# Kernel optimization log

Hardware: AMD Instinct MI355X
Metric: run time of the kernel (lower is better)

Reference implementation:

```python
import jax, jax.numpy as jnp
import numpy as np

P = 16            # patch_size
D = 256           # hidden_dim == P*P (required by final reshape)
H = 8             # num_heads
HD = D // H       # head_dim


def _sinusoid(n, d):
    # standard sinusoidal positional encoding, interleaved sin/cos
    pos = jnp.arange(n, dtype=jnp.float32)[:, None]            # (n,1)
    i = jnp.arange(0, d, 2, dtype=jnp.float32)                 # (d/2,)
    div = jnp.exp(-i * (jnp.log(10000.0) / d))                 # (d/2,)
    ang = pos * div                                            # (n, d/2)
    return jnp.stack([jnp.sin(ang), jnp.cos(ang)], axis=-1).reshape(n, d)


def _patch_embed(x, w, b):
    # Conv2d(in_ch, D, kernel=P, stride=P) then flatten to (B, N, D)
    e = jax.lax.conv_general_dilated(
        x, w, window_strides=(P, P), padding='VALID',
        dimension_numbers=('NCHW', 'OIHW', 'NCHW'))
    e = e + b[None, :, None, None]
    B = e.shape[0]
    e = e.reshape(B, D, -1).transpose(0, 2, 1)                 # (B, N, D)
    e = e + _sinusoid(e.shape[1], D)[None]                     # positional enc
    return e.reshape(B, -1, H, HD).transpose(0, 2, 1, 3)       # (B, H, N, HD)


def setup_inputs() -> dict:
    key = jax.random.key(0)
    ks = jax.random.split(key, 12)
    B = 16
    inp = {
        'q': jax.random.normal(ks[0], (B, 3, 512, 512), jnp.float32),
        'k': jax.random.normal(ks[1], (B, 3, 512, 512), jnp.float32),
        'v': jax.random.normal(ks[2], (B, 3, 512, 512), jnp.float32),
        'a': jax.random.normal(ks[3], (B, 3, 256, 256), jnp.float32),
    }
    s = 0.02
    for idx, name in enumerate('qkva'):
        inp['w' + name] = jax.random.normal(ks[4 + 2 * idx], (D, 3, P, P), jnp.float32) * s
        inp['b' + name] = jnp.zeros((D,), jnp.float32)
    return inp


def reference(q, k, v, a, wq, bq, wk, bk, wv, bv, wa, ba):
    qh = _patch_embed(q, wq, bq)   # (B,H,Nq,HD), Nq=1024
    kh = _patch_embed(k, wk, bk)   # (B,H,Nk,HD)
    vh = _patch_embed(v, wv, bv)   # (B,H,Nk,HD)
    ah = _patch_embed(a, wa, ba)   # (B,H,Na,HD), Na=256
    scale = HD ** -0.5
    # agent attention: two small softmax matmuls then Q @ (K @ V)
    Qs = jax.nn.softmax(jnp.einsum('bhnd,bhmd->bhnm', qh, ah) * scale, axis=-1)  # (B,H,Nq,Na)
    Ks = jax.nn.softmax(jnp.einsum('bhmd,bhnd->bhmn', ah, kh) * scale, axis=-1)  # (B,H,Na,Nk)
    KV = jnp.einsum('bhmn,bhnd->bhmd', Ks, vh)                                   # (B,H,Na,HD)
    A = jnp.einsum('bhnm,bhmd->bhnd', Qs, KV)                                    # (B,H,Nq,HD)
    B = A.shape[0]
    attn = A.transpose(0, 2, 1, 3).reshape(B, -1, D)            # (B, Nq, D)
    N = attn.shape[1]
    g = int(N ** 0.5)                                           # grid side (32)
    HW = g * P                                                  # 512
    attn = attn.reshape(B, N, P, P)
    attn = attn.reshape(B, g, g, P, P).transpose(0, 1, 3, 2, 4).reshape(B, HW, HW)
    return attn
```

## Files before the change

kernel.cpp:

```cpp
#include <hip/hip_runtime.h>
#include <cstdint>
#include <cstddef>

typedef __bf16 bf16x8 __attribute__((ext_vector_type(8)));
typedef __bf16 bf16x4 __attribute__((ext_vector_type(4)));
typedef float f32x4 __attribute__((ext_vector_type(4)));
typedef unsigned short u16x4 __attribute__((ext_vector_type(4)));
typedef unsigned short u16x8 __attribute__((ext_vector_type(8)));

#define MFMA16(a, b, c) __builtin_amdgcn_mfma_f32_16x16x32_bf16(a, b, c, 0, 0, 0)

__device__ __forceinline__ unsigned short f2bf(float f) {
    unsigned u = __builtin_bit_cast(unsigned, f);
    u = (u + 0x7FFFu + ((u >> 16) & 1u)) >> 16;
    return (unsigned short)u;
}

__global__ __launch_bounds__(256)
void prep(float* __restrict__ pe, unsigned short* __restrict__ Wb,
          const float* __restrict__ w0, const float* __restrict__ w1,
          const float* __restrict__ w2, const float* __restrict__ w3) {
    const int bx = blockIdx.x, t = threadIdx.x;
    if (bx < 1024) {
        int n = bx, d = t;
        int j = d >> 1;
        float div = expf(-(float)(2 * j) * 0.03597789207808881f);
        float ang = (float)n * div;
        pe[n * 256 + d] = (d & 1) ? cosf(ang) : sinf(ang);
    } else {
        int i = bx - 1024;
        int tensor = i / 192, blk = i - tensor * 192;
        const float* w = (tensor == 0) ? w0 : (tensor == 1) ? w1 : (tensor == 2) ? w2 : w3;
        int idx4 = blk * 256 + t;
        int d = idx4 / 192;
        int kq = (idx4 - d * 192) * 4;
        f32x4 v = *(const f32x4*)(w + (size_t)idx4 * 4);
        u16x4 o;
#pragma unroll
        for (int e = 0; e < 4; ++e) o[e] = f2bf(v[e]);
        unsigned short* dst = Wb + (size_t)tensor * 196608
                            + (d >> 4) * 12288 + (kq >> 5) * 512
                            + (d & 15) * 32 + (kq & 31);
        *(u16x4*)dst = o;
    }
}

struct EArgs {
    const float* src;
    const unsigned short* Wb;
    const float* bias;
    const float* pe;
    unsigned short* dst;
    int Np, lgNp, lgG, S, trans;
};

template<bool TR>
__device__ __forceinline__ void embed_body(const EArgs& A, int m0) {
    const int t = threadIdx.x, lane = t & 63, wid = t >> 6;
    const int l15 = lane & 15, l4 = lane >> 4;
    const int S = A.S;

    const float* pbase[4];
    int nn[4], bb[4];
#pragma unroll
    for (int j = 0; j < 4; ++j) {
        int p = m0 + j * 16 + l15;
        int b = p >> A.lgNp, n = p & (A.Np - 1);
        nn[j] = n; bb[j] = b;
        int gy = n >> A.lgG, gx = n & ((1 << A.lgG) - 1);
        pbase[j] = A.src + ((size_t)(b * 3) * S + gy * 16 + (l4 >> 1)) * (size_t)S
                 + gx * 16 + (l4 & 1) * 8;
    }
    const unsigned short* wbase = A.Wb + (size_t)(wid * 4) * 12288 + l15 * 32 + l4 * 8;

    f32x4 acc[4][4];
#pragma unroll
    for (int i = 0; i < 4; ++i)
#pragma unroll
        for (int j = 0; j < 4; ++j) acc[i][j] = f32x4{0.f, 0.f, 0.f, 0.f};

    for (int kt = 0; kt < 24; ++kt) {
        const size_t aoff = ((size_t)(kt >> 3) * S + (kt & 7) * 2) * (size_t)S;
        bf16x8 pf[4], wf[4];
#pragma unroll
        for (int j = 0; j < 4; ++j) {
            f32x4 lo = *(const f32x4*)(pbase[j] + aoff);
            f32x4 hi = *(const f32x4*)(pbase[j] + aoff + 4);
            bf16x8 v;
#pragma unroll
            for (int e = 0; e < 4; ++e) { v[e] = (__bf16)lo[e]; v[4 + e] = (__bf16)hi[e]; }
            pf[j] = v;
        }
#pragma unroll
        for (int i = 0; i < 4; ++i)
            wf[i] = *(const bf16x8*)(wbase + i * 12288 + kt * 512);
#pragma unroll
        for (int i = 0; i < 4; ++i)
#pragma unroll
            for (int j = 0; j < 4; ++j) {
                if (TR) acc[i][j] = MFMA16(pf[i], wf[j], acc[i][j]);
                else    acc[i][j] = MFMA16(wf[i], pf[j], acc[i][j]);
            }
    }

    if (!TR) {
#pragma unroll
        for (int i = 0; i < 4; ++i) {
            int d0 = wid * 64 + i * 16 + l4 * 4;
            int hh = d0 >> 5, hd = d0 & 31;
            f32x4 bs = *(const f32x4*)&A.bias[d0];
#pragma unroll
            for (int j = 0; j < 4; ++j) {
                int n = nn[j], b = bb[j];
                f32x4 pv = *(const f32x4*)&A.pe[n * 256 + d0];
                bf16x4 o;
#pragma unroll
                for (int r = 0; r < 4; ++r)
                    o[r] = (__bf16)(acc[i][j][r] + bs[r] + pv[r]);
                *(bf16x4*)&A.dst[(((size_t)(b * 8 + hh)) * A.Np + n) * 32 + hd] = o;
            }
        }
    } else {
#pragma unroll
        for (int j = 0; j < 4; ++j) {
            int d = wid * 64 + j * 16 + l15;
            int hh = d >> 5, hd = d & 31;
            float bsv = A.bias[d];
#pragma unroll
            for (int i = 0; i < 4; ++i) {
                int p0 = m0 + i * 16 + l4 * 4;
                int b = p0 >> A.lgNp, n0 = p0 & (A.Np - 1);
                bf16x4 o;
#pragma unroll
                for (int r = 0; r < 4; ++r)
                    o[r] = (__bf16)(acc[i][j][r] + bsv + A.pe[(n0 + r) * 256 + d]);
                *(bf16x4*)&A.dst[(((size_t)(b * 8 + hh)) * 32 + hd) * (size_t)A.Np + n0] = o;
            }
        }
    }
}

__global__ __launch_bounds__(256, 3)
void embed2(EArgs A0, EArgs A1, EArgs A2, EArgs A3) {
    const int bx = blockIdx.x;
    EArgs A; int m0;
    if      (bx < 256) { A = A0; m0 = bx * 64; }
    else if (bx < 512) { A = A1; m0 = (bx - 256) * 64; }
    else if (bx < 768) { A = A2; m0 = (bx - 512) * 64; }
    else               { A = A3; m0 = (bx - 768) * 64; }
    if (A.trans) embed_body<true>(A, m0);
    else         embed_body<false>(A, m0);
}

__global__ __launch_bounds__(512)
void s2kv_kernel(const unsigned short* __restrict__ ah_ws,
                 const unsigned short* __restrict__ kh_ws,
                 const unsigned short* __restrict__ vT_ws,
                 unsigned short* __restrict__ kvT_ws) {
    __shared__ unsigned short ahs[128][40];
    __shared__ unsigned short khs[128][40];
    __shared__ unsigned short vts[32][136];
    __shared__ unsigned short Ps[128][136];

    const int bid = blockIdx.x;
    const int half = bid & 1;
    const int h = (bid >> 1) & 7, b = bid >> 4;
    const int a0 = half * 128;
    const int t = threadIdx.x, lane = t & 63, wid = t >> 6;
    const int l15 = lane & 15, l4 = lane >> 4;
    const size_t bh = (size_t)(b * 8 + h);

    const unsigned short* ahp = ah_ws + (bh * 256 + a0) * 32;
    const unsigned short* khp = kh_ws + bh * 1024 * 32;
    const unsigned short* vtp = vT_ws + bh * 32 * 1024;

    {
        int row = t >> 2, kq = (t & 3) * 8;
        *(u16x8*)&ahs[row][kq] = *(const u16x8*)(ahp + row * 32 + kq);
    }
    __syncthreads();
    const bf16x8 af = *(const bf16x8*)&ahs[wid * 16 + l15][l4 * 8];

    const float scale = 0.17677669529663687f;
    float rs[4] = {0.f, 0.f, 0.f, 0.f};
    const f32x4 z = {0.f, 0.f, 0.f, 0.f};
    f32x4 kv[2];
    kv[0] = z; kv[1] = z;

    for (int kt = 0; kt < 8; ++kt) {
        const int n0 = kt * 128;
        __syncthreads();
        {
            int row = t >> 2, kq = (t & 3) * 8;
            *(u16x8*)&khs[row][kq] = *(const u16x8*)(khp + (size_t)(n0 + row) * 32 + kq);
        }
        {
            int row = t >> 4, cq = (t & 15) * 8;
            *(u16x8*)&vts[row][cq] = *(const u16x8*)(vtp + (size_t)row * 1024 + n0 + cq);
        }
        __syncthreads();
#pragma unroll
        for (int n16 = 0; n16 < 8; ++n16) {
            bf16x8 bfr = *(const bf16x8*)&khs[n16 * 16 + l15][l4 * 8];
            f32x4 s = MFMA16(af, bfr, z);
#pragma unroll
            for (int r = 0; r < 4; ++r) {
                float e = __expf(s[r] * scale);
                rs[r] += e;
                Ps[wid * 16 + l4 * 4 + r][n16 * 16 + l15] = f2bf(e);
            }
        }
        __syncthreads();
#pragma unroll
        for (int ks = 0; ks < 4; ++ks) {
            bf16x8 pa = *(const bf16x8*)&Ps[wid * 16 + l15][ks * 32 + l4 * 8];
#pragma unroll
            for (int n16 = 0; n16 < 2; ++n16) {
                bf16x8 vb = *(const bf16x8*)&vts[n16 * 16 + l15][ks * 32 + l4 * 8];
                kv[n16] = MFMA16(pa, vb, kv[n16]);
            }
        }
    }
#pragma unroll
    for (int r = 0; r < 4; ++r) {
        rs[r] += __shfl_xor(rs[r], 1, 64);
        rs[r] += __shfl_xor(rs[r], 2, 64);
        rs[r] += __shfl_xor(rs[r], 4, 64);
        rs[r] += __shfl_xor(rs[r], 8, 64);
    }
#pragma unroll
    for (int n16 = 0; n16 < 2; ++n16)
#pragma unroll
        for (int r = 0; r < 4; ++r) {
            int m = a0 + wid * 16 + l4 * 4 + r;
            int d = n16 * 16 + l15;
            kvT_ws[bh * 8192 + (size_t)d * 256 + m] = f2bf(kv[n16][r] / rs[r]);
        }
}

__global__ __launch_bounds__(256)
void qsa_kernel(const unsigned short* __restrict__ qh_ws,
                const unsigned short* __restrict__ ah_ws,
                const unsigned short* __restrict__ kvT_ws,
                float* __restrict__ out) {
    __shared__ unsigned short qhs[64][40];
    __shared__ unsigned short ahs[256][40];
    __shared__ unsigned short kvt[32][264];
    __shared__ unsigned short Ps[64][264];

    const int bid = blockIdx.x;
    const int qt = bid & 15, h = (bid >> 4) & 7, b = bid >> 7;
    const int m0 = qt * 64;
    const int t = threadIdx.x, lane = t & 63, wid = t >> 6;
    const int l15 = lane & 15, l4 = lane >> 4;
    const size_t bh = (size_t)(b * 8 + h);

    const unsigned short* qhp = qh_ws + (bh * 1024 + m0) * 32;
    const unsigned short* ahp = ah_ws + bh * 256 * 32;

    {
        int row = t >> 2, kq = (t & 3) * 8;
        *(u16x8*)&qhs[row][kq] = *(const u16x8*)(qhp + row * 32 + kq);
    }
    {
        *(u16x8*)&ahs[t][0]  = *(const u16x8*)(ahp + (size_t)t * 32);
        *(u16x8*)&ahs[t][8]  = *(const u16x8*)(ahp + (size_t)t * 32 + 8);
        *(u16x8*)&ahs[t][16] = *(const u16x8*)(ahp + (size_t)t * 32 + 16);
        *(u16x8*)&ahs[t][24] = *(const u16x8*)(ahp + (size_t)t * 32 + 24);
    }
#pragma unroll
    for (int i = 0; i < 4; ++i) {
        int chunk = t + i * 256;
        int row = chunk >> 5, cq = (chunk & 31) * 8;
        *(u16x8*)&kvt[row][cq] = *(const u16x8*)(kvT_ws + bh * 8192 + (size_t)row * 256 + cq);
    }
    __syncthreads();

    const bf16x8 qa = *(const bf16x8*)&qhs[wid * 16 + l15][l4 * 8];
    const float scale = 0.17677669529663687f;
    const f32x4 z = {0.f, 0.f, 0.f, 0.f};
    float rs[4] = {0.f, 0.f, 0.f, 0.f};
#pragma unroll
    for (int n16 = 0; n16 < 16; ++n16) {
        bf16x8 bfr = *(const bf16x8*)&ahs[n16 * 16 + l15][l4 * 8];
        f32x4 s = MFMA16(qa, bfr, z);
#pragma unroll
        for (int r = 0; r < 4; ++r) {
            float e = __expf(s[r] * scale);
            rs[r] += e;
            Ps[wid * 16 + l4 * 4 + r][n16 * 16 + l15] = f2bf(e);
        }
    }
#pragma unroll
    for (int r = 0; r < 4; ++r) {
        rs[r] += __shfl_xor(rs[r], 1, 64);
        rs[r] += __shfl_xor(rs[r], 2, 64);
        rs[r] += __shfl_xor(rs[r], 4, 64);
        rs[r] += __shfl_xor(rs[r], 8, 64);
    }
    __syncthreads();

    f32x4 o[2];
    o[0] = z; o[1] = z;
#pragma unroll
    for (int ks = 0; ks < 8; ++ks) {
        bf16x8 pa = *(const bf16x8*)&Ps[wid * 16 + l15][ks * 32 + l4 * 8];
#pragma unroll
        for (int n16 = 0; n16 < 2; ++n16) {
            bf16x8 kb = *(const bf16x8*)&kvt[n16 * 16 + l15][ks * 32 + l4 * 8];
            o[n16] = MFMA16(pa, kb, o[n16]);
        }
    }
#pragma unroll
    for (int n16 = 0; n16 < 2; ++n16) {
#pragma unroll
        for (int r = 0; r < 4; ++r) {
            int row = wid * 16 + l4 * 4 + r;
            int n = m0 + row;
            int gy = n >> 5, gx = n & 31;
            int hd = n16 * 16 + l15;
            int py = 2 * h + (hd >> 4), px = hd & 15;
            out[((size_t)b * 512 + gy * 16 + py) * 512 + gx * 16 + px] = o[n16][r] / rs[r];
        }
    }
}

extern "C" void kernel_launch(void* const* d_in, const int* in_sizes, int n_in,
                              void* d_out, int out_size, void* d_ws, size_t ws_size,
                              hipStream_t stream) {
    (void)in_sizes; (void)n_in; (void)out_size; (void)ws_size;

    const float* q  = (const float*)d_in[0];
    const float* k  = (const float*)d_in[1];
    const float* v  = (const float*)d_in[2];
    const float* a  = (const float*)d_in[3];
    const float* wq = (const float*)d_in[4];
    const float* bq = (const float*)d_in[5];
    const float* wk = (const float*)d_in[6];
    const float* bk = (const float*)d_in[7];
    const float* wv = (const float*)d_in[8];
    const float* bv = (const float*)d_in[9];
    const float* wa = (const float*)d_in[10];
    const float* ba = (const float*)d_in[11];
    float* out = (float*)d_out;

    char* ws = (char*)d_ws;
    float* pe           = (float*)(ws);
    unsigned short* Wb  = (unsigned short*)(ws + 1048576);
    unsigned short* kvT = (unsigned short*)(ws);
    unsigned short* qh  = (unsigned short*)(ws + 2621440);
    unsigned short* kh  = (unsigned short*)(ws + 11010048);
    unsigned short* ah  = (unsigned short*)(ws + 19398656);
    unsigned short* vT  = (unsigned short*)(ws + 21495808);

    prep<<<1792, 256, 0, stream>>>(pe, Wb, wq, wk, wv, wa);

    EArgs Aq = { q, Wb,              bq, pe, qh, 1024, 10, 5, 512, 0 };
    EArgs Ak = { k, Wb + 196608,     bk, pe, kh, 1024, 10, 5, 512, 0 };
    EArgs Av = { v, Wb + 2 * 196608, bv, pe, vT, 1024, 10, 5, 512, 1 };
    EArgs Aa = { a, Wb + 3 * 196608, ba, pe, ah,  256,  8, 4, 256, 0 };
    embed2<<<832, 256, 0, stream>>>(Aq, Ak, Av, Aa);

    s2kv_kernel<<<256, 512, 0, stream>>>(ah, kh, vT, kvT);
    qsa_kernel<<<2048, 256, 0, stream>>>(qh, ah, kvT, out);
}
```

Baseline: 126.6 us.

## Stage patch-embed input tiles through double-buffered LDS with prefetch

The patch-embedding GEMM now uses 128-patch by 128-channel tiles per block. Input pixels are loaded cooperatively with wide coalesced reads, converted to bf16 and written into a double-buffered shared-memory tile. Global loads run two k-steps ahead and weights one step ahead, so loads overlap the MFMA work. A transposed positional-encoding table is also precomputed so the transposed V epilogue can use vector loads. The cost is a __syncthreads per k-step, extra LDS use, and a larger prep kernel.

```diff
diff --git a/kernel.cpp b/kernel.cpp
--- a/kernel.cpp
+++ b/kernel.cpp
@@ -17,18 +17,29 @@
 }
 
 __global__ __launch_bounds__(256)
-void prep(float* __restrict__ pe, unsigned short* __restrict__ Wb,
+void prep(float* __restrict__ pe, float* __restrict__ peT, unsigned short* __restrict__ Wb,
           const float* __restrict__ w0, const float* __restrict__ w1,
           const float* __restrict__ w2, const float* __restrict__ w3) {
     const int bx = blockIdx.x, t = threadIdx.x;
+    const float LC = 0.03597789207808881f;
     if (bx < 1024) {
         int n = bx, d = t;
-        int j = d >> 1;
-        float div = expf(-(float)(2 * j) * 0.03597789207808881f);
+        float div = expf(-(float)(2 * (d >> 1)) * LC);
         float ang = (float)n * div;
         pe[n * 256 + d] = (d & 1) ? cosf(ang) : sinf(ang);
+    } else if (bx < 1280) {
+        int d = bx - 1024;
+        float div = expf(-(float)(2 * (d >> 1)) * LC);
+        f32x4 o;
+        int n0 = t * 4;
+#pragma unroll
+        for (int e = 0; e < 4; ++e) {
+            float ang = (float)(n0 + e) * div;
+            o[e] = (d & 1) ? cosf(ang) : sinf(ang);
+        }
+        *(f32x4*)&peT[(size_t)d * 1024 + n0] = o;
     } else {
-        int i = bx - 1024;
+        int i = bx - 1280;
         int tensor = i / 192, blk = i - tensor * 192;
         const float* w = (tensor == 0) ? w0 : (tensor == 1) ? w1 : (tensor == 2) ? w2 : w3;
         int idx4 = blk * 256 + t;
@@ -50,28 +61,55 @@
     const unsigned short* Wb;
     const float* bias;
     const float* pe;
+    const float* peT;
     unsigned short* dst;
     int Np, lgNp, lgG, S, trans;
 };
 
+typedef unsigned short AsTile[128][40];
+
 template<bool TR>
-__device__ __forceinline__ void embed_body(const EArgs& A, int m0) {
+__device__ __forceinline__ void embed_body(const EArgs& A, int m0, int nh, AsTile* As) {
     const int t = threadIdx.x, lane = t & 63, wid = t >> 6;
     const int l15 = lane & 15, l4 = lane >> 4;
+    const int wr = wid >> 1, wc = wid & 1;
     const int S = A.S;
 
-    const float* pbase[4];
-    int nn[4], bb[4];
-#pragma unroll
-    for (int j = 0; j < 4; ++j) {
-        int p = m0 + j * 16 + l15;
-        int b = p >> A.lgNp, n = p & (A.Np - 1);
-        nn[j] = n; bb[j] = b;
-        int gy = n >> A.lgG, gx = n & ((1 << A.lgG) - 1);
-        pbase[j] = A.src + ((size_t)(b * 3) * S + gy * 16 + (l4 >> 1)) * (size_t)S
-                 + gx * 16 + (l4 & 1) * 8;
-    }
-    const unsigned short* wbase = A.Wb + (size_t)(wid * 4) * 12288 + l15 * 32 + l4 * 8;
+    const int sp = t & 127;
+    const int sh = t >> 7;
+    {
+    }
+    int p_s = m0 + sp;
+    int b_s = p_s >> A.lgNp, n_s = p_s & (A.Np - 1);
+    int gy_s = n_s >> A.lgG, gx_s = n_s & ((1 << A.lgG) - 1);
+    const float* sbase = A.src + ((size_t)(b_s * 3) * S + gy_s * 16 + sh) * (size_t)S + gx_s * 16;
+
+    auto loadA = [&](int kt, f32x4* g) {
+        const float* a = sbase + ((size_t)(kt >> 3) * S + ((kt & 7) << 1)) * (size_t)S;
+        g[0] = *(const f32x4*)(a);
+        g[1] = *(const f32x4*)(a + 4);
+        g[2] = *(const f32x4*)(a + 8);
+        g[3] = *(const f32x4*)(a + 12);
+    };
+    auto writeA = [&](int buf, const f32x4* g) {
+        u16x8 o0, o1;
+#pragma unroll
+        for (int e = 0; e < 4; ++e) {
+            o0[e] = f2bf(g[0][e]); o0[4 + e] = f2bf(g[1][e]);
+            o1[e] = f2bf(g[2][e]); o1[4 + e] = f2bf(g[3][e]);
+        }
+        *(u16x8*)&As[buf][sp][sh * 16] = o0;
+        *(u16x8*)&As[buf][sp][sh * 16 + 8] = o1;
+    };
+
+    const unsigned short* wbase = A.Wb + (size_t)(nh * 8 + wc * 4) * 12288 + l15 * 32 + l4 * 8;
+    auto loadW = [&](int kt, bf16x8* wf) {
+#pragma unroll
+        for (int j = 0; j < 4; ++j) {
+            u16x8 r = *(const u16x8*)(wbase + j * 12288 + kt * 512);
+            wf[j] = __builtin_bit_cast(bf16x8, r);
+        }
+    };
 
     f32x4 acc[4][4];
 #pragma unroll
@@ -79,39 +117,52 @@
 #pragma unroll
         for (int j = 0; j < 4; ++j) acc[i][j] = f32x4{0.f, 0.f, 0.f, 0.f};
 
+    f32x4 gaA[4], gaB[4];
+    bf16x8 wfc[4];
+    loadA(0, gaA);
+    writeA(0, gaA);
+    loadA(1, gaA);
+    loadW(0, wfc);
+    __syncthreads();
+
+#pragma unroll 2
     for (int kt = 0; kt < 24; ++kt) {
-        const size_t aoff = ((size_t)(kt >> 3) * S + (kt & 7) * 2) * (size_t)S;
-        bf16x8 pf[4], wf[4];
+        const int c = kt & 1;
+        const int kA = (kt + 2 < 24) ? kt + 2 : 23;
+        const int kW = (kt + 1 < 24) ? kt + 1 : 23;
+        loadA(kA, gaB);
+        bf16x8 wfn[4];
+        loadW(kW, wfn);
+
+        bf16x8 pf[4];
+#pragma unroll
+        for (int i = 0; i < 4; ++i)
+            pf[i] = *(const bf16x8*)&As[c][wr * 64 + i * 16 + l15][l4 * 8];
+
+#pragma unroll
+        for (int i = 0; i < 4; ++i)
+#pragma unroll
+            for (int j = 0; j < 4; ++j) {
+                if (TR) acc[i][j] = MFMA16(pf[i], wfc[j], acc[i][j]);
+                else    acc[i][j] = MFMA16(wfc[j], pf[i], acc[i][j]);
+            }
+
+        writeA(c ^ 1, gaA);
+        __syncthreads();
+#pragma unroll
+        for (int j = 0; j < 4; ++j) { gaA[j] = gaB[j]; wfc[j] = wfn[j]; }
+    }
+
+    if (!TR) {
 #pragma unroll
         for (int j = 0; j < 4; ++j) {
-            f32x4 lo = *(const f32x4*)(pbase[j] + aoff);
-            f32x4 hi = *(const f32x4*)(pbase[j] + aoff + 4);
-            bf16x8 v;
-#pragma unroll
-            for (int e = 0; e < 4; ++e) { v[e] = (__bf16)lo[e]; v[4 + e] = (__bf16)hi[e]; }
-            pf[j] = v;
-        }
-#pragma unroll
-        for (int i = 0; i < 4; ++i)
-            wf[i] = *(const bf16x8*)(wbase + i * 12288 + kt * 512);
-#pragma unroll
-        for (int i = 0; i < 4; ++i)
-#pragma unroll
-            for (int j = 0; j < 4; ++j) {
-                if (TR) acc[i][j] = MFMA16(pf[i], wf[j], acc[i][j]);
-                else    acc[i][j] = MFMA16(wf[i], pf[j], acc[i][j]);
-            }
-    }
-
-    if (!TR) {
-#pragma unroll
-        for (int i = 0; i < 4; ++i) {
-            int d0 = wid * 64 + i * 16 + l4 * 4;
+            int d0 = nh * 128 + wc * 64 + j * 16 + l4 * 4;
             int hh = d0 >> 5, hd = d0 & 31;
             f32x4 bs = *(const f32x4*)&A.bias[d0];
 #pragma unroll
-            for (int j = 0; j < 4; ++j) {
-                int n = nn[j], b = bb[j];
+            for (int i = 0; i < 4; ++i) {
+                int p = m0 + wr * 64 + i * 16 + l15;
+                int b = p >> A.lgNp, n = p & (A.Np - 1);
                 f32x4 pv = *(const f32x4*)&A.pe[n * 256 + d0];
                 bf16x4 o;
 #pragma unroll
@@ -123,17 +174,18 @@
     } else {
 #pragma unroll
         for (int j = 0; j < 4; ++j) {
-            int d = wid * 64 + j * 16 + l15;
+            int d = nh * 128 + wc * 64 + j * 16 + l15;
             int hh = d >> 5, hd = d & 31;
             float bsv = A.bias[d];
 #pragma unroll
             for (int i = 0; i < 4; ++i) {
-                int p0 = m0 + i * 16 + l4 * 4;
+                int p0 = m0 + wr * 64 + i * 16 + l4 * 4;
                 int b = p0 >> A.lgNp, n0 = p0 & (A.Np - 1);
+                f32x4 pv = *(const f32x4*)&A.peT[(size_t)d * 1024 + n0];
                 bf16x4 o;
 #pragma unroll
                 for (int r = 0; r < 4; ++r)
-                    o[r] = (__bf16)(acc[i][j][r] + bsv + A.pe[(n0 + r) * 256 + d]);
+                    o[r] = (__bf16)(acc[i][j][r] + bsv + pv[r]);
                 *(bf16x4*)&A.dst[(((size_t)(b * 8 + hh)) * 32 + hd) * (size_t)A.Np + n0] = o;
             }
         }
@@ -141,15 +193,18 @@
 }
 
 __global__ __launch_bounds__(256, 3)
-void embed2(EArgs A0, EArgs A1, EArgs A2, EArgs A3) {
+void embed3(EArgs A0, EArgs A1, EArgs A2, EArgs A3) {
+    __shared__ unsigned short As[2][128][40];
     const int bx = blockIdx.x;
-    EArgs A; int m0;
-    if      (bx < 256) { A = A0; m0 = bx * 64; }
-    else if (bx < 512) { A = A1; m0 = (bx - 256) * 64; }
-    else if (bx < 768) { A = A2; m0 = (bx - 512) * 64; }
-    else               { A = A3; m0 = (bx - 768) * 64; }
-    if (A.trans) embed_body<true>(A, m0);
-    else         embed_body<false>(A, m0);
+    EArgs A; int lbx;
+    if      (bx < 256) { A = A0; lbx = bx; }
+    else if (bx < 512) { A = A1; lbx = bx - 256; }
+    else if (bx < 768) { A = A2; lbx = bx - 512; }
+    else               { A = A3; lbx = bx - 768; }
+    const int m0 = (lbx >> 1) * 128;
+    const int nh = lbx & 1;
+    if (A.trans) embed_body<true>(A, m0, nh, As);
+    else         embed_body<false>(A, m0, nh, As);
 }
 
 __global__ __launch_bounds__(512)
@@ -346,20 +401,21 @@
 
     char* ws = (char*)d_ws;
     float* pe           = (float*)(ws);
-    unsigned short* Wb  = (unsigned short*)(ws + 1048576);
+    float* peT          = (float*)(ws + 1048576);
+    unsigned short* Wb  = (unsigned short*)(ws + 2097152);
     unsigned short* kvT = (unsigned short*)(ws);
-    unsigned short* qh  = (unsigned short*)(ws + 2621440);
-    unsigned short* kh  = (unsigned short*)(ws + 11010048);
-    unsigned short* ah  = (unsigned short*)(ws + 19398656);
-    unsigned short* vT  = (unsigned short*)(ws + 21495808);
-
-    prep<<<1792, 256, 0, stream>>>(pe, Wb, wq, wk, wv, wa);
-
-    EArgs Aq = { q, Wb,              bq, pe, qh, 1024, 10, 5, 512, 0 };
-    EArgs Ak = { k, Wb + 196608,     bk, pe, kh, 1024, 10, 5, 512, 0 };
-    EArgs Av = { v, Wb + 2 * 196608, bv, pe, vT, 1024, 10, 5, 512, 1 };
-    EArgs Aa = { a, Wb + 3 * 196608, ba, pe, ah,  256,  8, 4, 256, 0 };
-    embed2<<<832, 256, 0, stream>>>(Aq, Ak, Av, Aa);
+    unsigned short* qh  = (unsigned short*)(ws + 3670016);
+    unsigned short* kh  = (unsigned short*)(ws + 12058624);
+    unsigned short* ah  = (unsigned short*)(ws + 20447232);
+    unsigned short* vT  = (unsigned short*)(ws + 22544384);
+
+    prep<<<2048, 256, 0, stream>>>(pe, peT, Wb, wq, wk, wv, wa);
+
+    EArgs Aq = { q, Wb,              bq, pe, peT, qh, 1024, 10, 5, 512, 0 };
+    EArgs Ak = { k, Wb + 196608,     bk, pe, peT, kh, 1024, 10, 5, 512, 0 };
+    EArgs Av = { v, Wb + 2 * 196608, bv, pe, peT, vT, 1024, 10, 5, 512, 1 };
+    EArgs Aa = { a, Wb + 3 * 196608, ba, pe, peT, ah,  256,  8, 4, 256, 0 };
+    embed3<<<832, 256, 0, stream>>>(Aq, Ak, Av, Aa);
 
     s2kv_kernel<<<256, 512, 0, stream>>>(ah, kh, vT, kvT);
     qsa_kernel<<<2048, 256, 0, stream>>>(qh, ah, kvT, out);
```

Measured after the change: 117.1 us. 7.5% less time.
